# Kernel optimization log

Measured on AMD Instinct MI355X. Metric: run time of the kernel, lower is better.

## Reference

```python
import jax, jax.numpy as jnp
import numpy as np

K = 7      # involution kernel size
G = 16     # groups
EPS = 1e-5 # BatchNorm eps (torch default)


def setup_inputs() -> dict:
    key = jax.random.key(0)
    ks = jax.random.split(key, 5)
    N, C, H, W = 4, 256, 56, 56
    Cr = C // 4            # ratio=4 reduction channels
    KKG = K * K * G        # 784 dynamic-kernel channels
    x = jax.random.normal(ks[0], (N, C, H, W), dtype=jnp.float32)
    w1 = jax.random.normal(ks[1], (Cr, C), dtype=jnp.float32) * 0.05
    b1 = jax.random.normal(ks[2], (Cr,), dtype=jnp.float32) * 0.05
    gamma = jnp.ones((Cr,), dtype=jnp.float32)
    beta = jnp.zeros((Cr,), dtype=jnp.float32)
    mean = jnp.zeros((Cr,), dtype=jnp.float32)
    var = jnp.ones((Cr,), dtype=jnp.float32)
    w2 = jax.random.normal(ks[3], (KKG, Cr), dtype=jnp.float32) * 0.05
    b2 = jax.random.normal(ks[4], (KKG,), dtype=jnp.float32) * 0.05
    return {"x": x, "w1": w1, "b1": b1, "gamma": gamma, "beta": beta,
            "mean": mean, "var": var, "w2": w2, "b2": b2}


def _involution(x, w1, b1, gamma, beta, mean, var, w2, b2):
    N, C, H, W = x.shape
    pad = K // 2
    # --- kernel-generating branch (stride=1 => AvgPool is identity) ---
    t = jnp.einsum('nchw,oc->nohw', x, w1) + b1[None, :, None, None]   # 1x1 conv
    inv_std = jax.lax.rsqrt(var + EPS)
    t = (t - mean[None, :, None, None]) * (inv_std * gamma)[None, :, None, None] \
        + beta[None, :, None, None]                                    # BatchNorm (inference)
    t = jax.nn.relu(t)
    ker = jnp.einsum('nohw,ko->nkhw', t, w2) + b2[None, :, None, None] # (N, K*K*G, H, W)
    ker = ker.reshape(N, G, K * K, H, W)                               # per-group dyn kernels
    # --- unfold (im2col), torch layout: (N, C, K*K, H, W), kk = kh*K + kw ---
    xp = jnp.pad(x, ((0, 0), (0, 0), (pad, pad), (pad, pad)))
    patches = jnp.stack(
        [xp[:, :, i:i + H, j:j + W] for i in range(K) for j in range(K)], axis=2)
    patches = patches.reshape(N, G, C // G, K * K, H, W)
    # --- per-pixel weighted sum over kernel positions ---
    out = jnp.einsum('ngckhw,ngkhw->ngchw', patches, ker)
    return out.reshape(N, C, H, W)


def reference(x, w1, b1, gamma, beta, mean, var, w2, b2):
    return _involution(x, w1, b1, gamma, beta, mean, var, w2, b2)
```

## Files before the change

kernel.cpp:

```cpp
#include <hip/hip_runtime.h>


#define CONST_AS __attribute__((address_space(4)))

namespace {
constexpr int Nn  = 4;
constexpr int Cc  = 256;
constexpr int Hh  = 56;
constexpr int Ww  = 56;
constexpr int HW  = Hh * Ww;
constexpr int NPX = Nn * HW;
constexpr int Cr  = 64;
constexpr int Gg  = 16;

constexpr size_t WS_W1F = 0;
constexpr size_t WS_BF  = WS_W1F + (size_t)Cc * Cr;
constexpr size_t WS_W2T = WS_BF  + Cr;
constexpr size_t WS_T   = WS_W2T + (size_t)Gg * 7 * Cr * 8;

__device__ __forceinline__ const CONST_AS float* cptr(const float* p) {
    return (const CONST_AS float*)(unsigned long long)p;
}
}

__global__ void __launch_bounds__(256)
k0_prep(const float* __restrict__ w1, const float* __restrict__ b1,
        const float* __restrict__ gamma, const float* __restrict__ beta,
        const float* __restrict__ mean,  const float* __restrict__ var,
        const float* __restrict__ w2,
        float* __restrict__ w1f, float* __restrict__ bf, float* __restrict__ w2t)
{
    const int id = blockIdx.x * 256 + threadIdx.x;
    if (id < Cc * Cr) {
        const int c = id / Cr, o = id - c * Cr;
        const float sc = gamma[o] * rsqrtf(var[o] + 1e-5f);
        w1f[id] = w1[o * Cc + c] * sc;
        if (id < Cr)
            bf[id] = fmaf(b1[id] - mean[id], gamma[id] * rsqrtf(var[id] + 1e-5f),
                          beta[id]);
    }
    if (id < Gg * 7 * Cr * 8) {
        const int g  = id / (7 * Cr * 8);
        const int r  = id - g * (7 * Cr * 8);
        const int kh = r / (Cr * 8);
        const int r2 = r - kh * (Cr * 8);
        const int o  = r2 >> 3;
        const int j  = r2 & 7;
        w2t[id] = (j < 7) ? w2[((g * 49 + kh * 7 + j)) * Cr + o] : 0.f;
    }
}

__global__ void __launch_bounds__(512)
k1_conv_bn_relu(const float* __restrict__ x, const float* __restrict__ w1f,
                const float* __restrict__ bf, float* __restrict__ t)
{
    __shared__ float xs[Cc][64];

    const int tid  = threadIdx.x;
    const int lane = tid & 63;
    const int q    = __builtin_amdgcn_readfirstlane(tid >> 6);
    const int tile = __builtin_amdgcn_readfirstlane((int)blockIdx.x);
    const int n    = __builtin_amdgcn_readfirstlane(tile / 49);
    const int hwb  = __builtin_amdgcn_readfirstlane((tile - n * 49) * 64);
    const int px   = tile * 64 + lane;

    const float* xb = x + (size_t)n * Cc * HW + hwb + lane;
    float v[32];
#pragma unroll
    for (int i = 0; i < 32; ++i)
        v[i] = xb[(size_t)(q + 8 * i) * HW];
#pragma unroll
    for (int i = 0; i < 32; ++i)
        xs[q + 8 * i][lane] = v[i];
    __syncthreads();

    const int o0 = q * 8;
    const CONST_AS float* wf = cptr(w1f) + o0;
    float acc[8];
#pragma unroll
    for (int i = 0; i < 8; ++i) acc[i] = 0.f;

#pragma unroll 4
    for (int c = 0; c < Cc; ++c) {
        const float xv = xs[c][lane];
        const CONST_AS float* wr = wf + c * Cr;
#pragma unroll
        for (int i = 0; i < 8; ++i)
            acc[i] = fmaf(xv, wr[i], acc[i]);
    }

    const CONST_AS float* bfc = cptr(bf) + o0;
#pragma unroll
    for (int i = 0; i < 8; ++i) {
        const float vv = acc[i] + bfc[i];
        t[(size_t)(o0 + i) * NPX + px] = vv > 0.f ? vv : 0.f;
    }
}

__global__ void __launch_bounds__(256)
k2_involution(const float* __restrict__ x, const float* __restrict__ t,
              const float* __restrict__ w2t, const float* __restrict__ b2,
              float* __restrict__ out)
{
    __shared__ float ts[Cr][64];
    __shared__ float red[4][16][64];

    const int lane = threadIdx.x & 63;
    const int wv   = __builtin_amdgcn_readfirstlane(threadIdx.x >> 6);
    const int tile = __builtin_amdgcn_readfirstlane((int)blockIdx.x);
    const int g    = __builtin_amdgcn_readfirstlane((int)blockIdx.y);
    const int n    = __builtin_amdgcn_readfirstlane(tile / 49);
    const int px   = tile * 64 + lane;
    const int hw   = px - n * HW;
    const int h    = hw / Ww;
    const int w    = hw - h * Ww;
    const int base = __builtin_amdgcn_readfirstlane(tile * 64 - n * HW);
    const int r0   = base / Ww;
    const int r1   = (base + 63) / Ww;

    {
        const float* tb = t + px;
        float v[16];
#pragma unroll
        for (int i = 0; i < 16; ++i)
            v[i] = tb[(size_t)(wv + 4 * i) * NPX];
#pragma unroll
        for (int i = 0; i < 16; ++i)
            ts[wv + 4 * i][lane] = v[i];
    }
    __syncthreads();

    float acc[16];
#pragma unroll
    for (int i = 0; i < 16; ++i) acc[i] = 0.f;

    const CONST_AS float* wg  = cptr(w2t) + (size_t)g * 7 * Cr * 8;
    const CONST_AS float* b2g = cptr(b2) + g * 49;
    const float* xg = x + (size_t)n * Cc * HW + (size_t)(g * 16) * HW;

#pragma unroll 1
    for (int s = 0; s < 2; ++s) {
        const int kh = wv + 4 * s;
        if (kh > 6) break;
        if (r1 + kh < 3 || r0 + kh - 3 >= Hh) continue;

        float ker[7];
#pragma unroll
        for (int j = 0; j < 7; ++j) ker[j] = b2g[kh * 7 + j];

        const CONST_AS float* wrow = wg + kh * (Cr * 8);
#pragma unroll 4
        for (int o = 0; o < Cr; ++o) {
            const float tc = ts[o][lane];
            const CONST_AS float* wr = wrow + o * 8;
#pragma unroll
            for (int j = 0; j < 7; ++j)
                ker[j] = fmaf(tc, wr[j], ker[j]);
        }

        const int hh = h + kh - 3;
        const bool hok = (hh >= 0) & (hh < Hh);
#pragma unroll 2
        for (int kw = 0; kw < 7; ++kw) {
            const int ww = w + kw - 3;
            const bool ok = hok & (ww >= 0) & (ww < Ww);
            const float kv = ok ? ker[kw] : 0.f;
            const int  off = ok ? hh * Ww + ww : 0;
            const float* xr = xg + off;
#pragma unroll
            for (int c = 0; c < 16; ++c)
                acc[c] = fmaf(xr[(size_t)c * HW], kv, acc[c]);
        }
    }

#pragma unroll
    for (int c = 0; c < 16; ++c)
        red[wv][c][lane] = acc[c];
    __syncthreads();

    float* og = out + (size_t)n * Cc * HW + (size_t)(g * 16) * HW + hw;
#pragma unroll
    for (int j = 0; j < 4; ++j) {
        const int c = wv * 4 + j;
        og[(size_t)c * HW] = red[0][c][lane] + red[1][c][lane]
                           + red[2][c][lane] + red[3][c][lane];
    }
}

extern "C" void kernel_launch(void* const* d_in, const int* in_sizes, int n_in,
                              void* d_out, int out_size, void* d_ws, size_t ws_size,
                              hipStream_t stream)
{
    const float* x     = (const float*)d_in[0];
    const float* w1    = (const float*)d_in[1];
    const float* b1    = (const float*)d_in[2];
    const float* gamma = (const float*)d_in[3];
    const float* beta  = (const float*)d_in[4];
    const float* mean  = (const float*)d_in[5];
    const float* var   = (const float*)d_in[6];
    const float* w2    = (const float*)d_in[7];
    const float* b2    = (const float*)d_in[8];

    float* ws  = (float*)d_ws;
    float* w1f = ws + WS_W1F;
    float* bf  = ws + WS_BF;
    float* w2t = ws + WS_W2T;
    float* t   = ws + WS_T;
    float* out = (float*)d_out;

    k0_prep<<<dim3(256), 256, 0, stream>>>(
        w1, b1, gamma, beta, mean, var, w2, w1f, bf, w2t);
    k1_conv_bn_relu<<<dim3(196), 512, 0, stream>>>(x, w1f, bf, t);
    k2_involution<<<dim3(196, Gg), 256, 0, stream>>>(x, t, w2t, b2, out);
}
```

Measured before the change: 98.22 us.

## Stage padded x halo tile in LDS and compute both kernel rows per wave

The involution kernel now loads a zero-padded 8-row halo of the 16 group channels into shared memory as float2 pairs, replacing per-tap global gathers with bounds checks. Each wave computes its two kernel-row weight sets in a single pass over interleaved t values. The cross-wave reduction goes through padded float4 shared-memory slots. The prep kernel is also rewritten so that its reads from w1 and w2 are coalesced. This cuts redundant global/L2 traffic and branching, at the cost of more LDS (48KB) and registers, which may lower occupancy.

```diff
diff --git a/kernel.cpp b/kernel.cpp
--- a/kernel.cpp
+++ b/kernel.cpp
@@ -32,21 +32,23 @@
 {
     const int id = blockIdx.x * 256 + threadIdx.x;
     if (id < Cc * Cr) {
-        const int c = id / Cr, o = id - c * Cr;
+        const int o = id >> 8, c = id & 255;
         const float sc = gamma[o] * rsqrtf(var[o] + 1e-5f);
-        w1f[id] = w1[o * Cc + c] * sc;
-        if (id < Cr)
-            bf[id] = fmaf(b1[id] - mean[id], gamma[id] * rsqrtf(var[id] + 1e-5f),
-                          beta[id]);
-    }
-    if (id < Gg * 7 * Cr * 8) {
-        const int g  = id / (7 * Cr * 8);
-        const int r  = id - g * (7 * Cr * 8);
-        const int kh = r / (Cr * 8);
-        const int r2 = r - kh * (Cr * 8);
-        const int o  = r2 >> 3;
-        const int j  = r2 & 7;
-        w2t[id] = (j < 7) ? w2[((g * 49 + kh * 7 + j)) * Cr + o] : 0.f;
+        w1f[c * Cr + o] = w1[id] * sc;
+    }
+    if (id < Cr)
+        bf[id] = fmaf(b1[id] - mean[id], gamma[id] * rsqrtf(var[id] + 1e-5f),
+                      beta[id]);
+    if (id < Gg * 49 * Cr) {
+        const int o = id & 63, kidx = id >> 6;
+        const int g = kidx / 49, r = kidx - g * 49;
+        const int kh = r / 7, j = r - kh * 7;
+        w2t[g * 3584 + kh * 512 + o * 8 + j] = w2[id];
+    }
+    if (id < Gg * 7 * Cr) {
+        const int g = id / 448, r = id - g * 448;
+        const int kh = r >> 6, o = r & 63;
+        w2t[g * 3584 + kh * 512 + o * 8 + 7] = 0.f;
     }
 }
 
@@ -102,21 +104,23 @@
               const float* __restrict__ w2t, const float* __restrict__ b2,
               float* __restrict__ out)
 {
-    __shared__ float ts[Cr][64];
-    __shared__ float red[4][16][64];
-
-    const int lane = threadIdx.x & 63;
-    const int wv   = __builtin_amdgcn_readfirstlane(threadIdx.x >> 6);
+    __shared__ __align__(16) float smem[12288];
+    float2* xs2 = (float2*)smem;
+    float*  tsw = smem + 8192;
+
+    const int tid  = threadIdx.x;
+    const int lane = tid & 63;
+    const int wv   = __builtin_amdgcn_readfirstlane(tid >> 6);
     const int tile = __builtin_amdgcn_readfirstlane((int)blockIdx.x);
     const int g    = __builtin_amdgcn_readfirstlane((int)blockIdx.y);
     const int n    = __builtin_amdgcn_readfirstlane(tile / 49);
+    const int base = __builtin_amdgcn_readfirstlane(tile * 64 - n * HW);
+    const int r0   = __builtin_amdgcn_readfirstlane(base / Ww);
     const int px   = tile * 64 + lane;
-    const int hw   = px - n * HW;
+    const int hw   = base + lane;
     const int h    = hw / Ww;
     const int w    = hw - h * Ww;
-    const int base = __builtin_amdgcn_readfirstlane(tile * 64 - n * HW);
-    const int r0   = base / Ww;
-    const int r1   = (base + 63) / Ww;
+    const int hrel = h - r0;
 
     {
         const float* tb = t + px;
@@ -125,66 +129,98 @@
         for (int i = 0; i < 16; ++i)
             v[i] = tb[(size_t)(wv + 4 * i) * NPX];
 #pragma unroll
-        for (int i = 0; i < 16; ++i)
-            ts[wv + 4 * i][lane] = v[i];
-    }
-    __syncthreads();
+        for (int i = 0; i < 16; ++i) {
+            const int o = wv + 4 * i;
+            tsw[(o >> 1) * 128 + lane * 2 + (o & 1)] = v[i];
+        }
+    }
+
+    {
+        const float* xgb = x + (size_t)n * Cc * HW + (size_t)(g * 16) * HW;
+#pragma unroll
+        for (int i = 0; i < 16; ++i) {
+            const int f   = tid + i * 256;
+            const int c2  = f >> 9;
+            const int rr  = (f >> 6) & 7;
+            const int col = f & 63;
+            const int hh  = r0 - 3 + rr;
+            const int cc  = col - 3;
+            const bool ok = (hh >= 0) & (hh < Hh) & (cc >= 0) & (cc < Ww);
+            const int off = ok ? (c2 * 2 * HW + hh * Ww + cc) : 0;
+            const float a = ok ? xgb[off] : 0.f;
+            const float b = ok ? xgb[off + HW] : 0.f;
+            xs2[f] = make_float2(a, b);
+        }
+    }
+    __syncthreads();
+
+    float ker[14];
+    {
+        const CONST_AS float* b2g = cptr(b2) + g * 49;
+        const int kh1 = (wv == 3) ? 6 : wv + 4;
+#pragma unroll
+        for (int j = 0; j < 7; ++j) {
+            ker[j]     = b2g[wv * 7 + j];
+            ker[7 + j] = b2g[kh1 * 7 + j];
+        }
+        const CONST_AS float* wg = cptr(w2t) + g * 3584;
+        const CONST_AS float* w0 = wg + wv * 512;
+        const CONST_AS float* w1r = wg + kh1 * 512;
+        const float2* tsp = (const float2*)tsw + lane;
+#pragma unroll 4
+        for (int o2 = 0; o2 < 32; ++o2) {
+            const float2 tv = tsp[o2 * 64];
+#pragma unroll
+            for (int j = 0; j < 7; ++j) {
+                ker[j]     = fmaf(tv.x, w0[o2 * 16 + j],      ker[j]);
+                ker[j]     = fmaf(tv.y, w0[o2 * 16 + 8 + j],  ker[j]);
+                ker[7 + j] = fmaf(tv.x, w1r[o2 * 16 + j],     ker[7 + j]);
+                ker[7 + j] = fmaf(tv.y, w1r[o2 * 16 + 8 + j], ker[7 + j]);
+            }
+        }
+    }
 
     float acc[16];
 #pragma unroll
     for (int i = 0; i < 16; ++i) acc[i] = 0.f;
 
-    const CONST_AS float* wg  = cptr(w2t) + (size_t)g * 7 * Cr * 8;
-    const CONST_AS float* b2g = cptr(b2) + g * 49;
-    const float* xg = x + (size_t)n * Cc * HW + (size_t)(g * 16) * HW;
-
-#pragma unroll 1
+#pragma unroll
     for (int s = 0; s < 2; ++s) {
-        const int kh = wv + 4 * s;
-        if (kh > 6) break;
-        if (r1 + kh < 3 || r0 + kh - 3 >= Hh) continue;
-
-        float ker[7];
-#pragma unroll
-        for (int j = 0; j < 7; ++j) ker[j] = b2g[kh * 7 + j];
-
-        const CONST_AS float* wrow = wg + kh * (Cr * 8);
-#pragma unroll 4
-        for (int o = 0; o < Cr; ++o) {
-            const float tc = ts[o][lane];
-            const CONST_AS float* wr = wrow + o * 8;
-#pragma unroll
-            for (int j = 0; j < 7; ++j)
-                ker[j] = fmaf(tc, wr[j], ker[j]);
-        }
-
-        const int hh = h + kh - 3;
-        const bool hok = (hh >= 0) & (hh < Hh);
-#pragma unroll 2
+        if (wv == 3 && s == 1) break;
+        const int row = hrel + wv + 4 * s;
+        const float2* xp = xs2 + row * 64 + w;
+        const int kb = s * 7;
+#pragma unroll
         for (int kw = 0; kw < 7; ++kw) {
-            const int ww = w + kw - 3;
-            const bool ok = hok & (ww >= 0) & (ww < Ww);
-            const float kv = ok ? ker[kw] : 0.f;
-            const int  off = ok ? hh * Ww + ww : 0;
-            const float* xr = xg + off;
-#pragma unroll
-            for (int c = 0; c < 16; ++c)
-                acc[c] = fmaf(xr[(size_t)c * HW], kv, acc[c]);
-        }
-    }
-
-#pragma unroll
-    for (int c = 0; c < 16; ++c)
-        red[wv][c][lane] = acc[c];
-    __syncthreads();
-
-    float* og = out + (size_t)n * Cc * HW + (size_t)(g * 16) * HW + hw;
-#pragma unroll
-    for (int j = 0; j < 4; ++j) {
-        const int c = wv * 4 + j;
-        og[(size_t)c * HW] = red[0][c][lane] + red[1][c][lane]
-                           + red[2][c][lane] + red[3][c][lane];
-    }
+            const float kv = ker[kb + kw];
+#pragma unroll
+            for (int c2 = 0; c2 < 8; ++c2) {
+                const float2 xv = xp[c2 * 512 + kw];
+                acc[2 * c2]     = fmaf(xv.x, kv, acc[2 * c2]);
+                acc[2 * c2 + 1] = fmaf(xv.y, kv, acc[2 * c2 + 1]);
+            }
+        }
+    }
+    __syncthreads();
+
+    float4* red4 = (float4*)smem;
+#pragma unroll
+    for (int q = 0; q < 4; ++q)
+        red4[(wv * 64 + lane) * 5 + q] =
+            make_float4(acc[4 * q], acc[4 * q + 1], acc[4 * q + 2], acc[4 * q + 3]);
+    __syncthreads();
+
+    float4 sum = red4[lane * 5 + wv];
+#pragma unroll
+    for (int q4 = 1; q4 < 4; ++q4) {
+        const float4 r = red4[(q4 * 64 + lane) * 5 + wv];
+        sum.x += r.x; sum.y += r.y; sum.z += r.z; sum.w += r.w;
+    }
+    float* og = out + (size_t)n * Cc * HW + (size_t)(g * 16 + wv * 4) * HW + hw;
+    og[0]              = sum.x;
+    og[(size_t)HW]     = sum.y;
+    og[(size_t)2 * HW] = sum.z;
+    og[(size_t)3 * HW] = sum.w;
 }
 
 extern "C" void kernel_launch(void* const* d_in, const int* in_sizes, int n_in,
```

Measured after the change: 118.3 us. 1.2x slower.
